# Optimization experiments

Measured on AMD Instinct MI355X. Metric: run time of the kernel, lower is better.

Reference implementation:

```python
import jax, jax.numpy as jnp
import numpy as np

D_MODEL = 1024
N_HEADS = 16
HEAD_DIM = D_MODEL // N_HEADS


def setup_inputs() -> dict:
    key = jax.random.key(0)
    ks = jax.random.split(key, 5)
    T, B = 2048, 2
    scale = 1.0 / np.sqrt(D_MODEL)
    x = jax.random.normal(ks[0], (T, B, D_MODEL), dtype=jnp.float32)
    W_qkv = jax.random.normal(ks[1], (D_MODEL, 3 * D_MODEL), dtype=jnp.float32) * scale
    b_qkv = jnp.zeros((3 * D_MODEL,), dtype=jnp.float32)
    W_out = jax.random.normal(ks[2], (D_MODEL, D_MODEL), dtype=jnp.float32) * scale
    b_out = jnp.zeros((D_MODEL,), dtype=jnp.float32)
    return {"x": x, "W_qkv": W_qkv, "b_qkv": b_qkv, "W_out": W_out, "b_out": b_out}


def reference(x, W_qkv, b_qkv, W_out, b_out):
    T, B, D = x.shape
    H, Dh = N_HEADS, HEAD_DIM
    qkv = x @ W_qkv + b_qkv  # [T, B, 3D]
    q, k, v = jnp.split(qkv, 3, axis=-1)
    # [T, B, D] -> [B, H, T, Dh]
    def to_heads(t):
        return t.reshape(T, B, H, Dh).transpose(1, 2, 0, 3)
    q, k, v = to_heads(q), to_heads(k), to_heads(v)
    scores = jnp.einsum("bhqd,bhkd->bhqk", q, k) / jnp.sqrt(jnp.float32(Dh))
    causal = jnp.tril(jnp.ones((T, T), dtype=bool))  # True where attention allowed
    scores = jnp.where(causal, scores, -jnp.inf)
    attn = jax.nn.softmax(scores, axis=-1)
    context = jnp.einsum("bhqk,bhkd->bhqd", attn, v)  # [B, H, T, Dh]
    context = context.transpose(2, 0, 1, 3).reshape(T, B, D)  # [T, B, D]
    return context @ W_out + b_out
```

## Files before the change

### kernel.cpp

```cpp
#include <hip/hip_runtime.h>
#include <stdint.h>

#define T_SEQ 2048
#define BATCH 2
#define DMODEL 1024
#define NH 16
#define DH 64
#define M_ROWS (T_SEQ * BATCH)
#define N_QKV (3 * DMODEL)
#define BHQ (32 * T_SEQ)

typedef unsigned short u16;
using bf16x8 = __attribute__((ext_vector_type(8))) __bf16;
using f32x4  = __attribute__((ext_vector_type(4))) float;

__device__ __forceinline__ u16 f2bf(float f) {
    union { float f; uint32_t u; } v; v.f = f;
    uint32_t r = v.u + 0x7fffu + ((v.u >> 16) & 1u);
    return (u16)(r >> 16);
}

__device__ __forceinline__ uint32_t pack2(float a, float b) {
    union { float f; uint32_t u; } x, y; x.f = a; y.f = b;
    return (x.u >> 16) | (y.u & 0xffff0000u);
}

__device__ __forceinline__ float bf2f(u16 u) {
    union { uint32_t u; float f; } v; v.u = (uint32_t)u << 16;
    return v.f;
}

__device__ __forceinline__ void lds_load16(void* lds, const void* g) {
    auto lp = (__attribute__((address_space(3))) uint32_t*)(uint32_t)(uintptr_t)lds;
    auto gp = (const __attribute__((address_space(1))) uint32_t*)(uintptr_t)g;
    __builtin_amdgcn_global_load_lds(gp, lp, 16, 0, 0);
}

#define SCQ 0.18033688011112f


__global__ void cvt4_kernel(const float* __restrict__ in, u16* __restrict__ out, int n4) {
    int i = blockIdx.x * 256 + threadIdx.x;
    if (i < n4) {
        float4 v = ((const float4*)in)[i];
        union { u16 u[4]; uint2 d; } o;
        o.u[0] = f2bf(v.x); o.u[1] = f2bf(v.y); o.u[2] = f2bf(v.z); o.u[3] = f2bf(v.w);
        ((uint2*)out)[i] = o.d;
    }
}

__global__ void cvt_t_kernel(const float* __restrict__ in, u16* __restrict__ out, int R, int C) {
    __shared__ float t[32][33];
    int bx = blockIdx.x * 32;
    int by = blockIdx.y * 32;
    int tx = threadIdx.x & 31, ty = threadIdx.x >> 5;
#pragma unroll
    for (int rr = 0; rr < 32; rr += 8)
        t[ty + rr][tx] = in[(size_t)(by + ty + rr) * C + bx + tx];
    __syncthreads();
#pragma unroll
    for (int rr = 0; rr < 32; rr += 8)
        out[(size_t)(bx + ty + rr) * R + by + tx] = f2bf(t[tx][ty + rr]);
}


template<int EPI>
__global__ __launch_bounds__(256) void gemm_kernel(
    const u16* __restrict__ A, const u16* __restrict__ Bt,
    const float* __restrict__ bias,
    u16* __restrict__ outQ, u16* __restrict__ outK, u16* __restrict__ outV,
    float* __restrict__ outF,
    int M, int N, int K)
{
    __shared__ __align__(16) u16 lA[128 * 32];
    __shared__ __align__(16) u16 lB[128 * 32];

    const int tid  = threadIdx.x;
    const int bm   = blockIdx.y * 128;
    const int bn   = blockIdx.x * 128;
    const int lane = tid & 63;
    const int wid  = tid >> 6;
    const int wm   = (wid >> 1) * 64;
    const int wn   = (wid & 1) * 64;
    const int qr   = lane & 15;
    const int quad = lane >> 4;
    const int r4   = lane >> 2;
    const int c4   = (((lane & 3) ^ ((r4 >> 1) & 3))) * 8;
    const int sw   = (qr >> 1) & 3;

    f32x4 acc[4][4];
#pragma unroll
    for (int i = 0; i < 4; i++)
#pragma unroll
        for (int j = 0; j < 4; j++) acc[i][j] = f32x4{0.f, 0.f, 0.f, 0.f};

    for (int k0 = 0; k0 < K; k0 += 32) {
        __syncthreads();
#pragma unroll
        for (int cc = 0; cc < 2; cc++) {
            int c = wid + cc * 4;
            lds_load16(&lA[c * 512], &A [(size_t)(bm + 16 * c + r4) * K + k0 + c4]);
            lds_load16(&lB[c * 512], &Bt[(size_t)(bn + 16 * c + r4) * K + k0 + c4]);
        }
        __syncthreads();

        bf16x8 af[4], bfr[4];
#pragma unroll
        for (int i = 0; i < 4; i++)
            af[i] = *(const bf16x8*)&lA[(wm + i * 16 + qr) * 32 + ((quad ^ sw) * 8)];
#pragma unroll
        for (int j = 0; j < 4; j++)
            bfr[j] = *(const bf16x8*)&lB[(wn + j * 16 + qr) * 32 + ((quad ^ sw) * 8)];
#pragma unroll
        for (int i = 0; i < 4; i++)
#pragma unroll
            for (int j = 0; j < 4; j++)
                acc[i][j] = __builtin_amdgcn_mfma_f32_16x16x32_bf16(af[i], bfr[j], acc[i][j], 0, 0, 0);
    }

#pragma unroll
    for (int i = 0; i < 4; i++) {
#pragma unroll
        for (int j = 0; j < 4; j++) {
            int col = bn + wn + j * 16 + qr;
            float bv = bias[col];
#pragma unroll
            for (int r = 0; r < 4; r++) {
                int row = bm + wm + i * 16 + quad * 4 + r;
                float val = acc[i][j][r] + bv;
                if (EPI == 0) {
                    int t = row >> 1, b = row & 1;
                    int which = col >> 10;
                    int dm = col & 1023;
                    int h = dm >> 6, dh = dm & 63;
                    int bh = b * NH + h;
                    if (which == 0) {
                        outQ[((size_t)bh * T_SEQ + t) * DH + dh] = f2bf(val * SCQ);
                    } else if (which == 1) {
                        outK[((size_t)bh * T_SEQ + t) * DH + dh] = f2bf(val);
                    } else {
                        outV[((size_t)bh * DH + dh) * T_SEQ + t] = f2bf(val);
                    }
                } else {
                    outF[(size_t)row * N + col] = val;
                }
            }
        }
    }
}


__global__ __launch_bounds__(256) void attn_kernel(
    const u16* __restrict__ Qb, const u16* __restrict__ Kb,
    const u16* __restrict__ Vt,
    u16* __restrict__ Op, float* __restrict__ Mp, float* __restrict__ Lp)
{
    __shared__ __align__(16) u16 lK[64 * 64];
    __shared__ __align__(16) u16 lV[64 * 64];
    __shared__ __align__(16) u16 lP[4][32 * 64];

    const int bh   = blockIdx.x;
    const int qt   = 15 - blockIdx.y;
    const int seg  = blockIdx.z;
    const int tid  = threadIdx.x;
    const int lane = tid & 63;
    const int wid  = tid >> 6;
    const int qr   = lane & 15;
    const int quad = lane >> 4;
    const int sw   = qr & 7;

    const int srow = wid * 8 + (lane >> 3);
    const int scol = (((lane & 7) ^ ((lane >> 3) & 7))) * 8;

    const u16* Q  = Qb + (size_t)bh * T_SEQ * DH;
    const u16* Kp = Kb + (size_t)bh * T_SEQ * DH;
    const u16* Vp = Vt + (size_t)bh * DH * T_SEQ;

    const int q0 = qt * 128 + wid * 32;

    bf16x8 qf[2][2];
#pragma unroll
    for (int g = 0; g < 2; g++)
#pragma unroll
        for (int ks = 0; ks < 2; ks++)
            qf[g][ks] = *(const bf16x8*)&Q[(size_t)(q0 + g * 16 + qr) * DH + ks * 32 + quad * 8];

    f32x4 o[2][4];
#pragma unroll
    for (int g = 0; g < 2; g++)
#pragma unroll
        for (int f = 0; f < 4; f++) o[g][f] = f32x4{0.f, 0.f, 0.f, 0.f};
    float m2[2] = {-1e30f, -1e30f}, l[2] = {0.f, 0.f};

    const int kt0 = seg ? qt + 1 : 0;
    const int kt1 = seg ? 2 * qt + 2 : qt + 1;

    for (int kt = kt0; kt < kt1; kt++) {
        __syncthreads();
#pragma unroll
        for (int half = 0; half < 2; half++) {
            lds_load16(&lK[half * 2048 + wid * 512],
                       &Kp[(size_t)(kt * 64 + half * 32 + srow) * DH + scol]);
            lds_load16(&lV[half * 2048 + wid * 512],
                       &Vp[(size_t)(half * 32 + srow) * T_SEQ + kt * 64 + scol]);
        }
        __syncthreads();

        if (kt * 64 > q0 + 31) continue;

        f32x4 s[2][4];
#pragma unroll
        for (int g = 0; g < 2; g++)
#pragma unroll
            for (int fn = 0; fn < 4; fn++) s[g][fn] = f32x4{0.f, 0.f, 0.f, 0.f};
#pragma unroll
        for (int fn = 0; fn < 4; fn++)
#pragma unroll
            for (int ks = 0; ks < 2; ks++) {
                bf16x8 kf = *(const bf16x8*)&lK[(fn * 16 + qr) * 64 + (((ks * 4 + quad) ^ sw) * 8)];
#pragma unroll
                for (int g = 0; g < 2; g++)
                    s[g][fn] = __builtin_amdgcn_mfma_f32_16x16x32_bf16(kf, qf[g][ks], s[g][fn], 0, 0, 0);
            }

        if (kt * 64 + 63 > q0) {
#pragma unroll
            for (int g = 0; g < 2; g++) {
                int q = q0 + g * 16 + qr;
#pragma unroll
                for (int fn = 0; fn < 4; fn++) {
                    int key = kt * 64 + fn * 16 + quad * 4;
#pragma unroll
                    for (int r = 0; r < 4; r++)
                        if (key + r > q) s[g][fn][r] = -1e30f;
                }
            }
        }

#pragma unroll
        for (int g = 0; g < 2; g++) {
            float mx = -1e30f;
#pragma unroll
            for (int fn = 0; fn < 4; fn++)
#pragma unroll
                for (int r = 0; r < 4; r++) mx = fmaxf(mx, s[g][fn][r]);
            mx = fmaxf(mx, __shfl_xor(mx, 16));
            mx = fmaxf(mx, __shfl_xor(mx, 32));
            float mnew  = fmaxf(m2[g], mx);
            float alpha = exp2f(m2[g] - mnew);
            m2[g] = mnew;

            float sum = 0.f;
#pragma unroll
            for (int fn = 0; fn < 4; fn++)
#pragma unroll
                for (int r = 0; r < 4; r++) {
                    union { float f; uint32_t u; } p;
                    p.f = exp2f(s[g][fn][r] - m2[g]);
                    p.u &= 0xffff0000u;
                    s[g][fn][r] = p.f;
                    sum += p.f;
                }
            sum += __shfl_xor(sum, 16);
            sum += __shfl_xor(sum, 32);
            l[g] = l[g] * alpha + sum;
#pragma unroll
            for (int f = 0; f < 4; f++)
#pragma unroll
                for (int r = 0; r < 4; r++) o[g][f][r] *= alpha;

#pragma unroll
            for (int fn = 0; fn < 4; fn++) {
                uint2 w; w.x = pack2(s[g][fn][0], s[g][fn][1]); w.y = pack2(s[g][fn][2], s[g][fn][3]);
                int phys = ((fn * 2 + (quad >> 1)) ^ sw);
                *(uint2*)&lP[wid][(g * 16 + qr) * 64 + phys * 8 + (quad & 1) * 4] = w;
            }
        }

        bf16x8 pf[2][2];
#pragma unroll
        for (int g = 0; g < 2; g++)
#pragma unroll
            for (int ks = 0; ks < 2; ks++)
                pf[g][ks] = *(const bf16x8*)&lP[wid][(g * 16 + qr) * 64 + (((ks * 4 + quad) ^ sw) * 8)];
#pragma unroll
        for (int f = 0; f < 4; f++)
#pragma unroll
            for (int ks = 0; ks < 2; ks++) {
                bf16x8 vf = *(const bf16x8*)&lV[(f * 16 + qr) * 64 + (((ks * 4 + quad) ^ sw) * 8)];
#pragma unroll
                for (int g = 0; g < 2; g++)
                    o[g][f] = __builtin_amdgcn_mfma_f32_16x16x32_bf16(vf, pf[g][ks], o[g][f], 0, 0, 0);
            }
    }

#pragma unroll
    for (int g = 0; g < 2; g++) {
        int q = q0 + g * 16 + qr;
        size_t rbase = (size_t)seg * BHQ + (size_t)bh * T_SEQ + q;
        if (quad == 0) { Mp[rbase] = m2[g]; Lp[rbase] = l[g]; }
#pragma unroll
        for (int f = 0; f < 4; f++) {
            uint2 w;
            w.x = (uint32_t)f2bf(o[g][f][0]) | ((uint32_t)f2bf(o[g][f][1]) << 16);
            w.y = (uint32_t)f2bf(o[g][f][2]) | ((uint32_t)f2bf(o[g][f][3]) << 16);
            *(uint2*)&Op[rbase * 64 + f * 16 + quad * 4] = w;
        }
    }
}


__global__ void merge_kernel(const u16* __restrict__ Op, const float* __restrict__ Mp,
                             const float* __restrict__ Lp, u16* __restrict__ ctx)
{
    int idx = blockIdx.x * 256 + threadIdx.x;
    int fq  = idx & 15;
    int q   = (idx >> 4) & (T_SEQ - 1);
    int bh  = idx >> 15;
    int b = bh >> 4, h = bh & 15;
    size_t rbase = (size_t)bh * T_SEQ + q;

    float m0 = Mp[rbase], m1 = Mp[rbase + BHQ];
    float l0 = Lp[rbase], l1 = Lp[rbase + BHQ];
    float m  = fmaxf(m0, m1);
    float w0 = exp2f(m0 - m), w1 = exp2f(m1 - m);
    float invl = 1.0f / (w0 * l0 + w1 * l1);
    w0 *= invl; w1 *= invl;

    union { uint2 d; u16 u[4]; } a, c, r;
    a.d = *(const uint2*)&Op[rbase * 64 + fq * 4];
    c.d = *(const uint2*)&Op[(rbase + BHQ) * 64 + fq * 4];
#pragma unroll
    for (int i = 0; i < 4; i++)
        r.u[i] = f2bf(w0 * bf2f(a.u[i]) + w1 * bf2f(c.u[i]));
    *(uint2*)&ctx[((size_t)q * BATCH + b) * DMODEL + h * DH + fq * 4] = r.d;
}


extern "C" void kernel_launch(void* const* d_in, const int* in_sizes, int n_in,
                              void* d_out, int out_size, void* d_ws, size_t ws_size,
                              hipStream_t stream) {
    const float* x     = (const float*)d_in[0];
    const float* W_qkv = (const float*)d_in[1];
    const float* b_qkv = (const float*)d_in[2];
    const float* W_out = (const float*)d_in[3];
    const float* b_out = (const float*)d_in[4];
    float* out = (float*)d_out;

    char* ws = (char*)d_ws;
    u16* xb     = (u16*)(ws + 0);
    u16* wqkv_t = (u16*)(ws + (8u  << 20));
    u16* wout_t = (u16*)(ws + (14u << 20));
    u16* Qb     = (u16*)(ws + (16u << 20));
    u16* Kb     = (u16*)(ws + (24u << 20));
    u16* Vt     = (u16*)(ws + (32u << 20));
    float* Mp   = (float*)(ws + (40u << 20));
    float* Lp   = (float*)(ws + (40u << 20) + (512u << 10));
    u16* ctx    = xb;
    u16* Op     = (u16*)d_out;

    cvt4_kernel <<<(M_ROWS * DMODEL / 4) / 256, 256, 0, stream>>>(x, xb, M_ROWS * DMODEL / 4);
    cvt_t_kernel<<<dim3(N_QKV / 32, DMODEL / 32), 256, 0, stream>>>(W_qkv, wqkv_t, DMODEL, N_QKV);
    cvt_t_kernel<<<dim3(DMODEL / 32, DMODEL / 32), 256, 0, stream>>>(W_out, wout_t, DMODEL, DMODEL);

    gemm_kernel<0><<<dim3(N_QKV / 128, M_ROWS / 128), 256, 0, stream>>>(
        xb, wqkv_t, b_qkv, Qb, Kb, Vt, nullptr, M_ROWS, N_QKV, DMODEL);

    attn_kernel<<<dim3(BATCH * NH, T_SEQ / 128, 2), 256, 0, stream>>>(Qb, Kb, Vt, Op, Mp, Lp);

    merge_kernel<<<(BHQ * 16) / 256, 256, 0, stream>>>(Op, Mp, Lp, ctx);

    gemm_kernel<1><<<dim3(DMODEL / 128, M_ROWS / 128), 256, 0, stream>>>(
        ctx, wout_t, b_out, nullptr, nullptr, nullptr, out, M_ROWS, DMODEL, DMODEL);
}
```

Measured before the change: 218.4 us.

## Generalize split-K attention to configurable segment count with multi-segment merge

The attention kernel now splits each query tile's key range into a configurable number of segments (4 when the workspace is large enough, otherwise 2) instead of a fixed two-way split at the diagonal. Partial outputs for segments 2-3 go to a second workspace buffer, and the merge kernel combines any number of segments using log-sum-exp weights. The aim is more blocks in flight and better occupancy on the many-CU GPU, at the cost of extra partial-output traffic and a heavier merge. It also drops the bf16 truncation mask applied to the softmax probabilities before summation, which slightly changes numerics.

```diff
diff --git a/kernel.cpp b/kernel.cpp
--- a/kernel.cpp
+++ b/kernel.cpp
@@ -153,7 +153,8 @@
 __global__ __launch_bounds__(256) void attn_kernel(
     const u16* __restrict__ Qb, const u16* __restrict__ Kb,
     const u16* __restrict__ Vt,
-    u16* __restrict__ Op, float* __restrict__ Mp, float* __restrict__ Lp)
+    u16* __restrict__ OpA, u16* __restrict__ OpB,
+    float* __restrict__ Mp, float* __restrict__ Lp, int segs)
 {
     __shared__ __align__(16) u16 lK[64 * 64];
     __shared__ __align__(16) u16 lV[64 * 64];
@@ -192,8 +193,9 @@
         for (int f = 0; f < 4; f++) o[g][f] = f32x4{0.f, 0.f, 0.f, 0.f};
     float m2[2] = {-1e30f, -1e30f}, l[2] = {0.f, 0.f};
 
-    const int kt0 = seg ? qt + 1 : 0;
-    const int kt1 = seg ? 2 * qt + 2 : qt + 1;
+    const int total = 2 * qt + 2;
+    const int kt0 = seg * total / segs;
+    const int kt1 = (seg + 1) * total / segs;
 
     for (int kt = kt0; kt < kt1; kt++) {
         __syncthreads();
@@ -255,11 +257,9 @@
             for (int fn = 0; fn < 4; fn++)
 #pragma unroll
                 for (int r = 0; r < 4; r++) {
-                    union { float f; uint32_t u; } p;
-                    p.f = exp2f(s[g][fn][r] - m2[g]);
-                    p.u &= 0xffff0000u;
-                    s[g][fn][r] = p.f;
-                    sum += p.f;
+                    float p = exp2f(s[g][fn][r] - m2[g]);
+                    s[g][fn][r] = p;
+                    sum += p;
                 }
             sum += __shfl_xor(sum, 16);
             sum += __shfl_xor(sum, 32);
@@ -294,11 +294,14 @@
             }
     }
 
+    u16* Op = (seg < 2) ? OpA : OpB;
+    const size_t sofs = (size_t)(seg & 1) * BHQ;
 #pragma unroll
     for (int g = 0; g < 2; g++) {
         int q = q0 + g * 16 + qr;
-        size_t rbase = (size_t)seg * BHQ + (size_t)bh * T_SEQ + q;
-        if (quad == 0) { Mp[rbase] = m2[g]; Lp[rbase] = l[g]; }
+        size_t rbase = sofs + (size_t)bh * T_SEQ + q;
+        size_t mlbase = (size_t)seg * BHQ + (size_t)bh * T_SEQ + q;
+        if (quad == 0) { Mp[mlbase] = m2[g]; Lp[mlbase] = l[g]; }
 #pragma unroll
         for (int f = 0; f < 4; f++) {
             uint2 w;
@@ -310,8 +313,9 @@
 }
 
 
-__global__ void merge_kernel(const u16* __restrict__ Op, const float* __restrict__ Mp,
-                             const float* __restrict__ Lp, u16* __restrict__ ctx)
+__global__ void merge_kernel(const u16* __restrict__ OpA, const u16* __restrict__ OpB,
+                             const float* __restrict__ Mp, const float* __restrict__ Lp,
+                             u16* __restrict__ ctx, int segs)
 {
     int idx = blockIdx.x * 256 + threadIdx.x;
     int fq  = idx & 15;
@@ -320,19 +324,24 @@
     int b = bh >> 4, h = bh & 15;
     size_t rbase = (size_t)bh * T_SEQ + q;
 
-    float m0 = Mp[rbase], m1 = Mp[rbase + BHQ];
-    float l0 = Lp[rbase], l1 = Lp[rbase + BHQ];
-    float m  = fmaxf(m0, m1);
-    float w0 = exp2f(m0 - m), w1 = exp2f(m1 - m);
-    float invl = 1.0f / (w0 * l0 + w1 * l1);
-    w0 *= invl; w1 *= invl;
-
-    union { uint2 d; u16 u[4]; } a, c, r;
-    a.d = *(const uint2*)&Op[rbase * 64 + fq * 4];
-    c.d = *(const uint2*)&Op[(rbase + BHQ) * 64 + fq * 4];
-#pragma unroll
-    for (int i = 0; i < 4; i++)
-        r.u[i] = f2bf(w0 * bf2f(a.u[i]) + w1 * bf2f(c.u[i]));
+    float m = -1e30f;
+    for (int s = 0; s < segs; s++) m = fmaxf(m, Mp[(size_t)s * BHQ + rbase]);
+    float denom = 0.f;
+    float acc[4] = {0.f, 0.f, 0.f, 0.f};
+    for (int s = 0; s < segs; s++) {
+        float w = exp2f(Mp[(size_t)s * BHQ + rbase] - m);
+        denom += w * Lp[(size_t)s * BHQ + rbase];
+        const u16* Op = (s < 2) ? OpA : OpB;
+        size_t ro = ((size_t)(s & 1) * BHQ + rbase) * 64 + fq * 4;
+        union { uint2 d; u16 u[4]; } a;
+        a.d = *(const uint2*)&Op[ro];
+#pragma unroll
+        for (int i = 0; i < 4; i++) acc[i] += w * bf2f(a.u[i]);
+    }
+    float invl = 1.0f / denom;
+    union { uint2 d; u16 u[4]; } r;
+#pragma unroll
+    for (int i = 0; i < 4; i++) r.u[i] = f2bf(acc[i] * invl);
     *(uint2*)&ctx[((size_t)q * BATCH + b) * DMODEL + h * DH + fq * 4] = r.d;
 }
 
@@ -355,9 +364,12 @@
     u16* Kb     = (u16*)(ws + (24u << 20));
     u16* Vt     = (u16*)(ws + (32u << 20));
     float* Mp   = (float*)(ws + (40u << 20));
-    float* Lp   = (float*)(ws + (40u << 20) + (512u << 10));
+    float* Lp   = (float*)(ws + (41u << 20));
     u16* ctx    = xb;
-    u16* Op     = (u16*)d_out;
+    u16* OpA    = (u16*)d_out;
+    u16* OpB    = (u16*)(ws + (48u << 20));
+
+    const int segs = (ws_size >= (64u << 20)) ? 4 : 2;
 
     cvt4_kernel <<<(M_ROWS * DMODEL / 4) / 256, 256, 0, stream>>>(x, xb, M_ROWS * DMODEL / 4);
     cvt_t_kernel<<<dim3(N_QKV / 32, DMODEL / 32), 256, 0, stream>>>(W_qkv, wqkv_t, DMODEL, N_QKV);
@@ -366,9 +378,10 @@
     gemm_kernel<0><<<dim3(N_QKV / 128, M_ROWS / 128), 256, 0, stream>>>(
         xb, wqkv_t, b_qkv, Qb, Kb, Vt, nullptr, M_ROWS, N_QKV, DMODEL);
 
-    attn_kernel<<<dim3(BATCH * NH, T_SEQ / 128, 2), 256, 0, stream>>>(Qb, Kb, Vt, Op, Mp, Lp);
-
-    merge_kernel<<<(BHQ * 16) / 256, 256, 0, stream>>>(Op, Mp, Lp, ctx);
+    attn_kernel<<<dim3(BATCH * NH, T_SEQ / 128, segs), 256, 0, stream>>>(
+        Qb, Kb, Vt, OpA, OpB, Mp, Lp, segs);
+
+    merge_kernel<<<(BHQ * 16) / 256, 256, 0, stream>>>(OpA, OpB, Mp, Lp, ctx, segs);
 
     gemm_kernel<1><<<dim3(DMODEL / 128, M_ROWS / 128), 256, 0, stream>>>(
         ctx, wout_t, b_out, nullptr, nullptr, nullptr, out, M_ROWS, DMODEL, DMODEL);
```

After: 221.4 us. About the same (+1.4%).
